# Optimization experiments

Measured on AMD Instinct MI355X. Metric: run time of the kernel, lower is better.

Reference implementation:

```python
import jax, jax.numpy as jnp
import numpy as np


def setup_inputs() -> dict:
    key = jax.random.key(0)
    ks = jax.random.split(key, 8)
    B, E, R, D, H = 8, 50000, 1000, 128, 256
    return {
        "head": jax.random.randint(ks[0], (B,), 0, E),
        "relation": jax.random.randint(ks[1], (B,), 0, R),
        "k": 10,
        "ent_emb": jax.random.normal(ks[2], (E, D), jnp.float32),
        "rel_emb": jax.random.normal(ks[3], (R, D), jnp.float32),
        "W1": jax.random.normal(ks[4], (3 * D, H), jnp.float32) * 0.05,
        "b1": jax.random.normal(ks[5], (H,), jnp.float32) * 0.05,
        "W2": jax.random.normal(ks[6], (H,), jnp.float32) * 0.05,
        "b2": jax.random.normal(ks[7], (1,), jnp.float32) * 0.05,
    }


def reference(head, relation, k, ent_emb, rel_emb, W1, b1, W2, b2):
    D = ent_emb.shape[1]
    # score_net first layer on cat([h, r, t]) == h@W1h + r@W1r + t@W1t (same math,
    # avoids materializing the [B*E, 3D] concat).
    W1h, W1r, W1t = W1[:D], W1[D:2 * D], W1[2 * D:]
    h = ent_emb[head]            # [B, D]
    r = rel_emb[relation]        # [B, D]
    ph = h @ W1h + r @ W1r + b1  # [B, H] -- head/relation part, computed once
    pt = ent_emb @ W1t           # [E, H] -- tail part over all entities
    hidden = jax.nn.relu(ph[:, None, :] + pt[None, :, :])   # [B, E, H]
    scores = jnp.einsum('beh,h->be', hidden, W2) + b2[0]     # [B, E]
    top_scores, top_indices = jax.lax.top_k(scores, k)
    return top_indices, top_scores
```

## Files before the change

kernel.cpp:

```cpp
#include <hip/hip_runtime.h>

#define D 128
#define HDIM 256
#define NB 8
#define NSHARD 16
#define CPS 16
#define NCAND (NSHARD * CPS)
#define PHW 16
#define WPAD 136

typedef short bf16x8 __attribute__((ext_vector_type(8)));
typedef float f32x4 __attribute__((ext_vector_type(4)));

__device__ __forceinline__ unsigned short f2bf(float x) {
    unsigned u = __float_as_uint(x);
    unsigned r = u + 0x7FFF + ((u >> 16) & 1);
    return (unsigned short)(r >> 16);
}
__device__ __forceinline__ bf16x8 pack_bf8(float4 u, float4 v) {
    union { bf16x8 v8; unsigned short s[8]; } r;
    r.s[0] = f2bf(u.x); r.s[1] = f2bf(u.y); r.s[2] = f2bf(u.z); r.s[3] = f2bf(u.w);
    r.s[4] = f2bf(v.x); r.s[5] = f2bf(v.y); r.s[6] = f2bf(v.z); r.s[7] = f2bf(v.w);
    return r.v8;
}

__device__ __forceinline__ unsigned long long sk_encode(float v, int idx) {
    unsigned u = __float_as_uint(v);
    u = (u & 0x80000000u) ? ~u : (u | 0x80000000u);
    return ((unsigned long long)u << 32) | (unsigned)(0xFFFFFFFFu - (unsigned)idx);
}
__device__ __forceinline__ float sk_val(unsigned long long key) {
    const unsigned u = (unsigned)(key >> 32);
    return (u & 0x80000000u) ? __uint_as_float(u & 0x7FFFFFFFu) : __uint_as_float(~u);
}
__device__ __forceinline__ int sk_idx(unsigned long long key) {
    return (int)(0xFFFFFFFFu - (unsigned)(key & 0xFFFFFFFFu));
}
__device__ __forceinline__ unsigned long long wave_max64(unsigned long long m) {
#pragma unroll
    for (int s = 32; s > 0; s >>= 1) {
        const unsigned long long o = __shfl_xor(m, s, 64);
        if (o > m) m = o;
    }
    return m;
}

__global__ __launch_bounds__(HDIM) void prep_kernel(
        const int* __restrict__ head, const int* __restrict__ relation,
        const float* __restrict__ ent_emb, const float* __restrict__ rel_emb,
        const float* __restrict__ W1, const float* __restrict__ b1,
        const float* __restrict__ W2, float* __restrict__ phW,
        unsigned short* __restrict__ w1tt) {
    const int w = blockIdx.x;
    const int tid = threadIdx.x;
    if (w < NB) {
        const int b = w;
        const long hidx = head[b];
        const long ridx = relation[b];
        const float* hrow = ent_emb + hidx * D;
        const float* rrow = rel_emb + ridx * D;
        float acc = b1[tid];
#pragma unroll 8
        for (int d = 0; d < D; ++d)
            acc += hrow[d] * W1[d * HDIM + tid];
#pragma unroll 8
        for (int d = 0; d < D; ++d)
            acc += rrow[d] * W1[(D + d) * HDIM + tid];
        phW[tid * PHW + b] = acc;
        if (b == 0) phW[tid * PHW + 8] = W2[tid];
    } else {
        const int k0 = (w - NB) * 4;
        const float* w1t = W1 + 2 * D * HDIM;
        unsigned short pk[4];
#pragma unroll
        for (int j = 0; j < 4; ++j)
            pk[j] = f2bf(w1t[(k0 + j) * HDIM + tid]);
        *(ushort4*)(w1tt + tid * D + k0) = make_ushort4(pk[0], pk[1], pk[2], pk[3]);
    }
}

__global__ __launch_bounds__(512, 4) void score_kernel(
        const float* __restrict__ ent_emb, const unsigned short* __restrict__ w1tt,
        const float* __restrict__ phW, float* __restrict__ scores, int E) {
    __shared__ __align__(16) unsigned short wL[HDIM][WPAD];
    __shared__ float phB[NB][HDIM];
    __shared__ float w2L[HDIM];

    const int tid = threadIdx.x;
    const int lane = tid & 63;
    const int wave = tid >> 6;
    const int lm = lane & 15;
    const int q = lane >> 4;
    const int base_e = blockIdx.x * 128 + wave * 16;

    const float* arow = ent_emb + (size_t)min(base_e + lm, E - 1) * D;
    bf16x8 aF[4];
#pragma unroll
    for (int kk = 0; kk < 4; ++kk) {
        const float4 u = *(const float4*)(arow + kk * 32 + q * 8);
        const float4 v = *(const float4*)(arow + kk * 32 + q * 8 + 4);
        aF[kk] = pack_bf8(u, v);
    }

#pragma unroll
    for (int i = 0; i < 8; ++i) {
        const int c = i * 512 + tid;
        const int row = c >> 4;
        const int col = (c & 15) << 3;
        *(uint4*)(&wL[row][col]) = *(const uint4*)(w1tt + row * D + col);
    }
    if (tid < HDIM) {
        const float4 p0 = *(const float4*)(phW + tid * PHW);
        const float4 p1 = *(const float4*)(phW + tid * PHW + 4);
        phB[0][tid] = p0.x; phB[1][tid] = p0.y; phB[2][tid] = p0.z; phB[3][tid] = p0.w;
        phB[4][tid] = p1.x; phB[5][tid] = p1.y; phB[6][tid] = p1.z; phB[7][tid] = p1.w;
        w2L[tid] = phW[tid * PHW + 8];
    }
    __syncthreads();

    float sp[NB * 4];
#pragma unroll
    for (int i = 0; i < NB * 4; ++i) sp[i] = 0.f;

#pragma unroll
    for (int t = 0; t < 16; ++t) {
        const int h = t * 16 + lm;
        bf16x8 bF[4];
#pragma unroll
        for (int kk = 0; kk < 4; ++kk)
            bF[kk] = *(const bf16x8*)(&wL[h][kk * 32 + q * 8]);

        float phv[8];
#pragma unroll
        for (int b = 0; b < NB; ++b) phv[b] = phB[b][h];
        const float w2v = w2L[h];

        f32x4 acc = (f32x4){0.f, 0.f, 0.f, 0.f};
#pragma unroll
        for (int kk = 0; kk < 4; ++kk)
            acc = __builtin_amdgcn_mfma_f32_16x16x32_bf16(aF[kk], bF[kk], acc, 0, 0, 0);

#pragma unroll
        for (int b = 0; b < NB; ++b)
#pragma unroll
            for (int r = 0; r < 4; ++r)
                sp[b * 4 + r] += fmaxf(phv[b] + acc[r], 0.f) * w2v;
    }

#pragma unroll
    for (int m = 1; m <= 8; m <<= 1) {
#pragma unroll
        for (int i = 0; i < NB * 4; ++i)
            sp[i] += __shfl_xor(sp[i], m, 64);
    }
    if (lm == 0) {
#pragma unroll
        for (int r = 0; r < 4; ++r) {
            const int e = base_e + q * 4 + r;
            if (e < E) {
#pragma unroll
                for (int b = 0; b < NB; ++b)
                    scores[(size_t)b * E + e] = sp[b * 4 + r];
            }
        }
    }
}

__global__ __launch_bounds__(256) void topk_rescore_kernel(
        const float* __restrict__ scores, int E,
        const float* __restrict__ ent_emb, const float* __restrict__ W1,
        const float* __restrict__ phW, const float* __restrict__ b2,
        unsigned long long* __restrict__ cand_exact) {
    const int b = blockIdx.x >> 4;
    const int s = blockIdx.x & 15;
    const int tid = threadIdx.x;
    const int lane = tid & 63;
    const int wave = tid >> 6;

    __shared__ unsigned long long cl[4 * CPS];
    __shared__ unsigned long long candk[CPS];
    __shared__ int eIdxs[CPS];
    __shared__ float entR[CPS][D];
    __shared__ float red[4][CPS];

    {
        const int shard = (E + NSHARD - 1) / NSHARD;
        const int start = s * shard;
        const int end = min(E, start + shard);
        const float* row = scores + (size_t)b * E;

        unsigned long long keys[CPS];
#pragma unroll
        for (int i = 0; i < CPS; ++i) keys[i] = 0ull;

        for (int e = start + tid; e < end; e += 256) {
            unsigned long long key = sk_encode(row[e], e);
            if (key > keys[CPS - 1]) {
#pragma unroll
                for (int j = 0; j < CPS; ++j) {
                    const bool gt = key > keys[j];
                    const unsigned long long mx = gt ? key : keys[j];
                    key = gt ? keys[j] : key;
                    keys[j] = mx;
                }
            }
        }
        for (int r = 0; r < CPS; ++r) {
            const unsigned long long m = wave_max64(keys[0]);
            if (keys[0] == m) {
#pragma unroll
                for (int j = 0; j < CPS - 1; ++j) keys[j] = keys[j + 1];
                keys[CPS - 1] = 0ull;
            }
            if (lane == 0) cl[wave * CPS + r] = m;
        }
        __syncthreads();
        if (wave == 0) {
            unsigned long long v = cl[lane];
            for (int r = 0; r < CPS; ++r) {
                const unsigned long long m = wave_max64(v);
                if (v == m) v = 0ull;
                if (lane == 0) candk[r] = m;
            }
        }
        __syncthreads();
    }

    if (tid < CPS) eIdxs[tid] = sk_idx(candk[tid]);
    __syncthreads();
    for (int t = tid; t < CPS * (D / 4); t += 256) {
        const int row = t >> 5, c4 = (t & 31) * 4;
        *(float4*)(&entR[row][c4]) =
            *(const float4*)(ent_emb + (size_t)eIdxs[row] * D + c4);
    }
    __syncthreads();

    const float* w1t = W1 + 2 * D * HDIM;
    float acc[CPS];
#pragma unroll
    for (int c = 0; c < CPS; ++c) acc[c] = 0.f;
    for (int d0 = 0; d0 < D; d0 += 4) {
        float w[4];
#pragma unroll
        for (int j = 0; j < 4; ++j) w[j] = w1t[(d0 + j) * HDIM + tid];
#pragma unroll
        for (int c = 0; c < CPS; ++c) {
            const float4 f = *(const float4*)(&entR[c][d0]);
            acc[c] += f.x * w[0] + f.y * w[1] + f.z * w[2] + f.w * w[3];
        }
    }
    const float phv = phW[tid * PHW + b];
    const float w2v = phW[tid * PHW + 8];
    float sc[CPS];
#pragma unroll
    for (int c = 0; c < CPS; ++c) sc[c] = fmaxf(acc[c] + phv, 0.f) * w2v;

#pragma unroll
    for (int m = 1; m <= 32; m <<= 1)
#pragma unroll
        for (int c = 0; c < CPS; ++c) sc[c] += __shfl_xor(sc[c], m, 64);
    if (lane == 0)
#pragma unroll
        for (int c = 0; c < CPS; ++c) red[wave][c] = sc[c];
    __syncthreads();
    if (tid < CPS) {
        const float v = red[0][tid] + red[1][tid] + red[2][tid] + red[3][tid] + b2[0];
        cand_exact[(size_t)(b * NSHARD + s) * CPS + tid] = sk_encode(v, eIdxs[tid]);
    }
}

__global__ __launch_bounds__(256) void final_kernel(
        const unsigned long long* __restrict__ cand_exact, int k,
        float* __restrict__ out) {
    const int lane = threadIdx.x & 63;
    const int wave = threadIdx.x >> 6;
    for (int b = wave; b < NB; b += 4) {
        unsigned long long lk[4];
#pragma unroll
        for (int j = 0; j < 4; ++j)
            lk[j] = cand_exact[(size_t)b * NCAND + j * 64 + lane];
#pragma unroll
        for (int i = 0; i < 4; ++i)
#pragma unroll
            for (int j = 0; j < 3; ++j)
                if (lk[j] < lk[j + 1]) {
                    const unsigned long long t = lk[j];
                    lk[j] = lk[j + 1];
                    lk[j + 1] = t;
                }
        for (int r = 0; r < k; ++r) {
            const unsigned long long m = wave_max64(lk[0]);
            if (lk[0] == m) {
#pragma unroll
                for (int j = 0; j < 3; ++j) lk[j] = lk[j + 1];
                lk[3] = 0ull;
            }
            if (lane == 0) {
                out[b * k + r] = (float)sk_idx(m);
                out[NB * k + b * k + r] = sk_val(m);
            }
        }
    }
}

extern "C" void kernel_launch(void* const* d_in, const int* in_sizes, int n_in,
                              void* d_out, int out_size, void* d_ws, size_t ws_size,
                              hipStream_t stream) {
    const int*   head     = (const int*)d_in[0];
    const int*   relation = (const int*)d_in[1];
    const float* ent_emb  = (const float*)d_in[3];
    const float* rel_emb  = (const float*)d_in[4];
    const float* W1       = (const float*)d_in[5];
    const float* b1       = (const float*)d_in[6];
    const float* W2       = (const float*)d_in[7];
    const float* b2       = (const float*)d_in[8];

    const int B = in_sizes[0];
    const int E = in_sizes[3] / D;
    int k = out_size / (2 * B);
    if (k > CPS) k = CPS;

    char* ws = (char*)d_ws;
    unsigned long long* cand_exact = (unsigned long long*)ws;
    float*          phW       = (float*)(ws + 16384);
    unsigned short* w1tt      = (unsigned short*)(ws + 32768);
    float*          scores    = (float*)(ws + 98304);
    float*          out       = (float*)d_out;

    prep_kernel<<<NB + 32, HDIM, 0, stream>>>(head, relation, ent_emb, rel_emb,
                                              W1, b1, W2, phW, w1tt);
    const int nblk = (E + 127) / 128;
    score_kernel<<<nblk, 512, 0, stream>>>(ent_emb, w1tt, phW, scores, E);
    topk_rescore_kernel<<<NB * NSHARD, 256, 0, stream>>>(
        scores, E, ent_emb, W1, phW, b2, cand_exact);
    final_kernel<<<1, 256, 0, stream>>>(cand_exact, k, out);
}
```

Baseline: 155.6 us.

## Fuse per-block top-16 selection into score kernel and merge rescore with final top-k

The score kernel now keeps its 128x8 block scores in shared memory and writes only each block's top-16 candidates per batch row, instead of the full B×E score matrix. A single merge kernel per batch row then selects the top 32 from all block candidates, rescores them exactly in fp32, and writes the final top-k. This replaces the old sharded top-k kernel plus final kernel and removes one launch and the full score-matrix round trip. In exchange only 8 blocks do the merge, each scanning about 6k candidates, so that stage has little parallelism.

```diff
diff --git a/kernel.cpp b/kernel.cpp
--- a/kernel.cpp
+++ b/kernel.cpp
@@ -1,13 +1,13 @@
 #include <hip/hip_runtime.h>
+#include <float.h>
 
 #define D 128
 #define HDIM 256
 #define NB 8
-#define NSHARD 16
-#define CPS 16
-#define NCAND (NSHARD * CPS)
 #define PHW 16
 #define WPAD 136
+#define CPB 16
+#define RESC 32
 
 typedef short bf16x8 __attribute__((ext_vector_type(8)));
 typedef float f32x4 __attribute__((ext_vector_type(4)));
@@ -81,7 +81,8 @@
 
 __global__ __launch_bounds__(512, 4) void score_kernel(
         const float* __restrict__ ent_emb, const unsigned short* __restrict__ w1tt,
-        const float* __restrict__ phW, float* __restrict__ scores, int E) {
+        const float* __restrict__ phW, unsigned long long* __restrict__ cand,
+        int E, int nblk) {
     __shared__ __align__(16) unsigned short wL[HDIM][WPAD];
     __shared__ float phB[NB][HDIM];
     __shared__ float w2L[HDIM];
@@ -153,151 +154,164 @@
         for (int i = 0; i < NB * 4; ++i)
             sp[i] += __shfl_xor(sp[i], m, 64);
     }
+
+    __syncthreads();
+    float* scL = (float*)&wL[0][0];
     if (lm == 0) {
 #pragma unroll
         for (int r = 0; r < 4; ++r) {
-            const int e = base_e + q * 4 + r;
-            if (e < E) {
-#pragma unroll
-                for (int b = 0; b < NB; ++b)
-                    scores[(size_t)b * E + e] = sp[b * 4 + r];
-            }
-        }
-    }
-}
-
-__global__ __launch_bounds__(256) void topk_rescore_kernel(
-        const float* __restrict__ scores, int E,
+            const int slot = wave * 16 + q * 4 + r;
+            const bool ok = (base_e + q * 4 + r) < E;
+#pragma unroll
+            for (int b = 0; b < NB; ++b)
+                scL[b * 128 + slot] = ok ? sp[b * 4 + r] : -FLT_MAX;
+        }
+    }
+    __syncthreads();
+
+    {
+        const int row = wave;
+        const int e0 = blockIdx.x * 128 + lane;
+        const int e1 = blockIdx.x * 128 + 64 + lane;
+        unsigned long long k0 = sk_encode(scL[row * 128 + lane], e0);
+        unsigned long long k1 = sk_encode(scL[row * 128 + 64 + lane], e1);
+        if (k1 > k0) { const unsigned long long t = k0; k0 = k1; k1 = t; }
+        unsigned long long* crow = cand + (size_t)row * nblk * CPB + blockIdx.x * CPB;
+        for (int r = 0; r < CPB; ++r) {
+            const unsigned long long m = wave_max64(k0);
+            if (k0 == m) { k0 = k1; k1 = 0ull; }
+            if (lane == 0) crow[r] = m;
+        }
+    }
+}
+
+__global__ __launch_bounds__(512) void merge_rescore_kernel(
+        const unsigned long long* __restrict__ cand, int nblk,
         const float* __restrict__ ent_emb, const float* __restrict__ W1,
         const float* __restrict__ phW, const float* __restrict__ b2,
-        unsigned long long* __restrict__ cand_exact) {
-    const int b = blockIdx.x >> 4;
-    const int s = blockIdx.x & 15;
+        int E, int k, float* __restrict__ out) {
+    const int row = blockIdx.x;
     const int tid = threadIdx.x;
     const int lane = tid & 63;
     const int wave = tid >> 6;
 
-    __shared__ unsigned long long cl[4 * CPS];
-    __shared__ unsigned long long candk[CPS];
-    __shared__ int eIdxs[CPS];
-    __shared__ float entR[CPS][D];
-    __shared__ float red[4][CPS];
+    __shared__ __align__(16) float entL[RESC][D];
+    __shared__ unsigned long long wTop[8 * RESC];
+    __shared__ unsigned long long candTop[RESC];
+    __shared__ int eIdx[RESC];
+    __shared__ float red[8][16];
+    __shared__ float exCand[RESC];
 
     {
-        const int shard = (E + NSHARD - 1) / NSHARD;
-        const int start = s * shard;
-        const int end = min(E, start + shard);
-        const float* row = scores + (size_t)b * E;
-
-        unsigned long long keys[CPS];
-#pragma unroll
-        for (int i = 0; i < CPS; ++i) keys[i] = 0ull;
-
-        for (int e = start + tid; e < end; e += 256) {
-            unsigned long long key = sk_encode(row[e], e);
-            if (key > keys[CPS - 1]) {
-#pragma unroll
-                for (int j = 0; j < CPS; ++j) {
-                    const bool gt = key > keys[j];
-                    const unsigned long long mx = gt ? key : keys[j];
-                    key = gt ? keys[j] : key;
-                    keys[j] = mx;
+        const int ncand = nblk * CPB;
+        const unsigned long long* crow = cand + (size_t)row * ncand;
+        unsigned long long lk[16];
+#pragma unroll
+        for (int i = 0; i < 16; ++i) lk[i] = 0ull;
+        for (int t = tid; t < ncand; t += 512) {
+            unsigned long long key = crow[t];
+            if (key > lk[15]) {
+#pragma unroll
+                for (int j = 0; j < 16; ++j) {
+                    const bool gt = key > lk[j];
+                    const unsigned long long mx = gt ? key : lk[j];
+                    key = gt ? lk[j] : key;
+                    lk[j] = mx;
                 }
             }
         }
-        for (int r = 0; r < CPS; ++r) {
-            const unsigned long long m = wave_max64(keys[0]);
-            if (keys[0] == m) {
-#pragma unroll
-                for (int j = 0; j < CPS - 1; ++j) keys[j] = keys[j + 1];
-                keys[CPS - 1] = 0ull;
+        for (int r = 0; r < RESC; ++r) {
+            const unsigned long long m = wave_max64(lk[0]);
+            if (lk[0] == m) {
+#pragma unroll
+                for (int j = 0; j < 15; ++j) lk[j] = lk[j + 1];
+                lk[15] = 0ull;
             }
-            if (lane == 0) cl[wave * CPS + r] = m;
+            if (lane == 0) wTop[wave * RESC + r] = m;
         }
         __syncthreads();
         if (wave == 0) {
-            unsigned long long v = cl[lane];
-            for (int r = 0; r < CPS; ++r) {
-                const unsigned long long m = wave_max64(v);
-                if (v == m) v = 0ull;
-                if (lane == 0) candk[r] = m;
+            unsigned long long m4[4];
+#pragma unroll
+            for (int j = 0; j < 4; ++j) m4[j] = wTop[j * 64 + lane];
+#pragma unroll
+            for (int i = 0; i < 4; ++i)
+#pragma unroll
+                for (int j = 0; j < 3; ++j)
+                    if (m4[j] < m4[j + 1]) {
+                        const unsigned long long t = m4[j];
+                        m4[j] = m4[j + 1];
+                        m4[j + 1] = t;
+                    }
+            for (int r = 0; r < RESC; ++r) {
+                const unsigned long long m = wave_max64(m4[0]);
+                if (m4[0] == m) {
+#pragma unroll
+                    for (int j = 0; j < 3; ++j) m4[j] = m4[j + 1];
+                    m4[3] = 0ull;
+                }
+                if (lane == 0) candTop[r] = m;
             }
         }
         __syncthreads();
     }
 
-    if (tid < CPS) eIdxs[tid] = sk_idx(candk[tid]);
-    __syncthreads();
-    for (int t = tid; t < CPS * (D / 4); t += 256) {
-        const int row = t >> 5, c4 = (t & 31) * 4;
-        *(float4*)(&entR[row][c4]) =
-            *(const float4*)(ent_emb + (size_t)eIdxs[row] * D + c4);
-    }
-    __syncthreads();
-
+    if (tid < RESC) eIdx[tid] = min(sk_idx(candTop[tid]), E - 1);
+    __syncthreads();
+    for (int t = tid; t < RESC * (D / 4); t += 512) {
+        const int r = t >> 5, c4 = (t & 31) * 4;
+        *(float4*)(&entL[r][c4]) =
+            *(const float4*)(ent_emb + (size_t)eIdx[r] * D + c4);
+    }
+    __syncthreads();
+
+    const int h = tid & 255;
+    const int cbase = (tid < 256) ? 0 : 16;
     const float* w1t = W1 + 2 * D * HDIM;
-    float acc[CPS];
-#pragma unroll
-    for (int c = 0; c < CPS; ++c) acc[c] = 0.f;
+    float acc[16];
+#pragma unroll
+    for (int c = 0; c < 16; ++c) acc[c] = 0.f;
     for (int d0 = 0; d0 < D; d0 += 4) {
         float w[4];
 #pragma unroll
-        for (int j = 0; j < 4; ++j) w[j] = w1t[(d0 + j) * HDIM + tid];
-#pragma unroll
-        for (int c = 0; c < CPS; ++c) {
-            const float4 f = *(const float4*)(&entR[c][d0]);
+        for (int j = 0; j < 4; ++j) w[j] = w1t[(d0 + j) * HDIM + h];
+#pragma unroll
+        for (int c = 0; c < 16; ++c) {
+            const float4 f = *(const float4*)(&entL[cbase + c][d0]);
             acc[c] += f.x * w[0] + f.y * w[1] + f.z * w[2] + f.w * w[3];
         }
     }
-    const float phv = phW[tid * PHW + b];
-    const float w2v = phW[tid * PHW + 8];
-    float sc[CPS];
-#pragma unroll
-    for (int c = 0; c < CPS; ++c) sc[c] = fmaxf(acc[c] + phv, 0.f) * w2v;
+    const float phv = phW[h * PHW + row];
+    const float w2v = phW[h * PHW + 8];
+    float sc[16];
+#pragma unroll
+    for (int c = 0; c < 16; ++c) sc[c] = fmaxf(acc[c] + phv, 0.f) * w2v;
 
 #pragma unroll
     for (int m = 1; m <= 32; m <<= 1)
 #pragma unroll
-        for (int c = 0; c < CPS; ++c) sc[c] += __shfl_xor(sc[c], m, 64);
+        for (int c = 0; c < 16; ++c) sc[c] += __shfl_xor(sc[c], m, 64);
     if (lane == 0)
 #pragma unroll
-        for (int c = 0; c < CPS; ++c) red[wave][c] = sc[c];
-    __syncthreads();
-    if (tid < CPS) {
-        const float v = red[0][tid] + red[1][tid] + red[2][tid] + red[3][tid] + b2[0];
-        cand_exact[(size_t)(b * NSHARD + s) * CPS + tid] = sk_encode(v, eIdxs[tid]);
-    }
-}
-
-__global__ __launch_bounds__(256) void final_kernel(
-        const unsigned long long* __restrict__ cand_exact, int k,
-        float* __restrict__ out) {
-    const int lane = threadIdx.x & 63;
-    const int wave = threadIdx.x >> 6;
-    for (int b = wave; b < NB; b += 4) {
-        unsigned long long lk[4];
-#pragma unroll
-        for (int j = 0; j < 4; ++j)
-            lk[j] = cand_exact[(size_t)b * NCAND + j * 64 + lane];
-#pragma unroll
-        for (int i = 0; i < 4; ++i)
-#pragma unroll
-            for (int j = 0; j < 3; ++j)
-                if (lk[j] < lk[j + 1]) {
-                    const unsigned long long t = lk[j];
-                    lk[j] = lk[j + 1];
-                    lk[j + 1] = t;
-                }
+        for (int c = 0; c < 16; ++c) red[wave][c] = sc[c];
+    __syncthreads();
+    if (tid < RESC) {
+        const int half = tid >> 4;
+        const int c = tid & 15;
+        exCand[tid] = red[half * 4 + 0][c] + red[half * 4 + 1][c]
+                    + red[half * 4 + 2][c] + red[half * 4 + 3][c] + b2[0];
+    }
+    __syncthreads();
+
+    if (wave == 0) {
+        unsigned long long key = (lane < RESC)
+            ? sk_encode(exCand[lane], eIdx[lane]) : 0ull;
         for (int r = 0; r < k; ++r) {
-            const unsigned long long m = wave_max64(lk[0]);
-            if (lk[0] == m) {
-#pragma unroll
-                for (int j = 0; j < 3; ++j) lk[j] = lk[j + 1];
-                lk[3] = 0ull;
-            }
+            const unsigned long long m = wave_max64(key);
+            if (key == m) key = 0ull;
             if (lane == 0) {
-                out[b * k + r] = (float)sk_idx(m);
-                out[NB * k + b * k + r] = sk_val(m);
+                out[row * k + r] = (float)sk_idx(m);
+                out[NB * k + row * k + r] = sk_val(m);
             }
         }
     }
@@ -318,20 +332,19 @@
     const int B = in_sizes[0];
     const int E = in_sizes[3] / D;
     int k = out_size / (2 * B);
-    if (k > CPS) k = CPS;
+    if (k > CPB) k = CPB;
 
     char* ws = (char*)d_ws;
-    unsigned long long* cand_exact = (unsigned long long*)ws;
-    float*          phW       = (float*)(ws + 16384);
-    unsigned short* w1tt      = (unsigned short*)(ws + 32768);
-    float*          scores    = (float*)(ws + 98304);
-    float*          out       = (float*)d_out;
+    unsigned long long* cand = (unsigned long long*)ws;
+    float*          phW      = (float*)(ws + 524288);
+    unsigned short* w1tt     = (unsigned short*)(ws + 540672);
+    float*          out      = (float*)d_out;
+
+    const int nblk = (E + 127) / 128;
 
     prep_kernel<<<NB + 32, HDIM, 0, stream>>>(head, relation, ent_emb, rel_emb,
                                               W1, b1, W2, phW, w1tt);
-    const int nblk = (E + 127) / 128;
-    score_kernel<<<nblk, 512, 0, stream>>>(ent_emb, w1tt, phW, scores, E);
-    topk_rescore_kernel<<<NB * NSHARD, 256, 0, stream>>>(
-        scores, E, ent_emb, W1, phW, b2, cand_exact);
-    final_kernel<<<1, 256, 0, stream>>>(cand_exact, k, out);
-}
+    score_kernel<<<nblk, 512, 0, stream>>>(ent_emb, w1tt, phW, cand, E, nblk);
+    merge_rescore_kernel<<<NB, 512, 0, stream>>>(cand, nblk, ent_emb, W1, phW,
+                                                 b2, E, k, out);
+}
```

Result: slower. 311.9 us (+100.5%).
